# Performance work log

Hardware: AMD Instinct MI355X
Metric: run time of the kernel (lower is better)

## Reference

```python
import jax, jax.numpy as jnp
import numpy as np

B, S, D, H, K = 16, 4096, 256, 512, 3
EPS = 1e-5


def setup_inputs() -> dict:
    key = jax.random.key(0)
    ks = jax.random.split(key, 16)
    glorot = lambda k, shape: jax.random.uniform(
        k, shape, jnp.float32, -1.0, 1.0) * np.sqrt(6.0 / (shape[0] + shape[-1]))
    return {
        "inputs": jax.random.normal(ks[0], (B, S, D), jnp.float32),
        "mask": jax.random.randint(ks[1], (B, S), 0, 2, jnp.int32),
        "in_w": glorot(ks[2], (H, D)),
        "in_b": jnp.zeros((H,), jnp.float32),
        "gate_w": glorot(ks[3], (H, D)),
        "gate_b": jnp.zeros((H,), jnp.float32),
        "dw_w": glorot(ks[4], (H, 1, K)),
        "dw_b": jnp.zeros((H,), jnp.float32),
        "pw_w": glorot(ks[5], (H, H, 1)),
        "pw_b": jnp.zeros((H,), jnp.float32),
        "ln_g": jnp.ones((H,), jnp.float32),
        "ln_b": jnp.zeros((H,), jnp.float32),
        "A_log": jax.random.normal(ks[6], (H,), jnp.float32) * -0.1,
        "Bp": jax.random.normal(ks[7], (H,), jnp.float32) * 0.1,
        "Cp": jax.random.normal(ks[8], (H,), jnp.float32) * 0.1,
    }


def _forward(inputs, mask, in_w, in_b, gate_w, gate_b, dw_w, dw_b,
             pw_w, pw_b, ln_g, ln_b, A_log, Bp, Cp):
    # projections: torch Linear is x @ W.T + b
    x_lin = jnp.einsum('bsd,hd->bsh', inputs, in_w) + in_b
    g_lin = jnp.einsum('bsd,hd->bsh', inputs, gate_w) + gate_b
    h = jnp.tanh(x_lin)
    m_f = mask.astype(h.dtype)                      # [B,S]
    h = h * m_f[:, :, None]
    # depthwise conv over time: [B,H,S] with groups=H, 'same' padding
    pad = (K - 1) // 2
    h_t = jnp.transpose(h, (0, 2, 1))               # [B,H,S]
    h_conv = jax.lax.conv_general_dilated(
        h_t, dw_w, window_strides=(1,), padding=[(pad, pad)],
        dimension_numbers=('NCH', 'OIH', 'NCH'), feature_group_count=H)
    h_conv = h_conv + dw_b[None, :, None]
    h_conv = jnp.transpose(h_conv, (0, 2, 1))       # [B,S,H]
    # pointwise 1x1 conv
    h_conv = jnp.einsum('bsh,oh->bso', h_conv, pw_w[:, :, 0]) + pw_b
    u = jax.nn.silu(h_conv + h)
    g = jax.nn.sigmoid(g_lin)
    a_exp = jnp.exp(-jax.nn.softplus(A_log))        # [H]

    def step(carry, xs):
        state, last = carry
        ut, gt, mt = xs                             # [B,H],[B,H],[B]
        new_state = gt * (a_exp * state) + (1.0 - gt) * (Bp * ut)
        keep = (mt > 0.5)[:, None]
        state = jnp.where(keep, new_state, state)
        y = state * Cp
        last = jnp.where(keep, y, last)
        return (state, last), last

    init = (jnp.zeros((B, H), u.dtype), jnp.zeros((B, H), u.dtype))
    xs = (jnp.transpose(u, (1, 0, 2)), jnp.transpose(g, (1, 0, 2)),
          jnp.transpose(m_f, (1, 0)))
    _, y_seq = jax.lax.scan(step, init, xs)         # [S,B,H]
    y_seq = jnp.transpose(y_seq, (1, 0, 2))         # [B,S,H]
    # LayerNorm over last dim
    mu = jnp.mean(y_seq, axis=-1, keepdims=True)
    var = jnp.var(y_seq, axis=-1, keepdims=True)
    return (y_seq - mu) * jax.lax.rsqrt(var + EPS) * ln_g + ln_b


def reference(inputs, mask, in_w, in_b, gate_w, gate_b, dw_w, dw_b,
              pw_w, pw_b, ln_g, ln_b, A_log, Bp, Cp):
    return _forward(inputs, mask, in_w, in_b, gate_w, gate_b, dw_w, dw_b,
                    pw_w, pw_b, ln_g, ln_b, A_log, Bp, Cp)
```

## Files before the change

### kernel.cpp

```cpp
#include <hip/hip_runtime.h>
#include <hip/hip_bf16.h>
#include <math.h>

#define B_  16
#define S_  4096
#define D_  256
#define H_  512
#define BS_ 65536
#define BSH_ 33554432L
#define BSD_ 16777216L
#define CCH 128
#define LCH 32
#define TPAD 136

typedef __bf16 bf16;
typedef __bf16 bf16x8 __attribute__((ext_vector_type(8)));
typedef float  f32x4  __attribute__((ext_vector_type(4)));

#define AS1 __attribute__((address_space(1)))
#define AS3 __attribute__((address_space(3)))

__device__ __forceinline__ void gload_lds16(const void* g, void* l) {
  __builtin_amdgcn_global_load_lds((const AS1 void*)g, (AS3 void*)l, 16, 0, 0);
}

#if __has_builtin(__builtin_amdgcn_exp2f)
#define EXP2F __builtin_amdgcn_exp2f
#else
#define EXP2F exp2f
#endif
#if __has_builtin(__builtin_amdgcn_rcpf)
#define RCPF __builtin_amdgcn_rcpf
#else
#define RCPF(x) (1.f/(x))
#endif
#define L2E 1.4426950408889634f

__device__ __forceinline__ float fsigmoid(float x) {
  return RCPF(1.f + EXP2F(-L2E * x));
}
__device__ __forceinline__ float ftanh(float x) {
  return 2.f * RCPF(1.f + EXP2F(-2.f * L2E * x)) - 1.f;
}
__device__ __forceinline__ float fsilu(float x) {
  return x * RCPF(1.f + EXP2F(-L2E * x));
}

__global__ void k_cast_x(const float* __restrict__ x, bf16* __restrict__ xb, int n8) {
  int i = blockIdx.x * blockDim.x + threadIdx.x;
  if (i >= n8) return;
  const float4* p = (const float4*)x + (long)i * 2;
  float4 a = p[0], b = p[1];
  bf16x8 o;
  o[0]=(bf16)a.x; o[1]=(bf16)a.y; o[2]=(bf16)a.z; o[3]=(bf16)a.w;
  o[4]=(bf16)b.x; o[5]=(bf16)b.y; o[6]=(bf16)b.z; o[7]=(bf16)b.w;
  ((bf16x8*)xb)[i] = o;
}

__global__ void k_cast_w(const float* __restrict__ in_w, const float* __restrict__ gate_w,
                         const float* __restrict__ pw_w,
                         bf16* __restrict__ w1, bf16* __restrict__ pw) {
  int i = blockIdx.x * blockDim.x + threadIdx.x;
  const int HD = H_ * D_;
  if (i < HD)            w1[i] = (bf16)in_w[i];
  else if (i < 2 * HD)   w1[i] = (bf16)gate_w[i - HD];
  else {
    int j = i - 2 * HD;
    if (j < H_ * H_)     pw[j] = (bf16)pw_w[j];
  }
}

template<int KDIM, int EPI>
__global__ __launch_bounds__(256)
void k_gemm(const bf16* __restrict__ A, const bf16* __restrict__ Bw,
            const int* __restrict__ mask,
            const float* __restrict__ bias0, const float* __restrict__ bias1,
            const bf16* __restrict__ hbuf,
            bf16* __restrict__ out0, bf16* __restrict__ out1, int Ntiles)
{
  extern __shared__ char smem_raw[];
  bf16* As_ = (bf16*)smem_raw;
  bf16* Bs_ = (bf16*)smem_raw + 3 * 4096;
  bf16* tile = (bf16*)smem_raw;

  const int t = threadIdx.x;
  const int w = t >> 6, lane = t & 63;
  const int nwg = gridDim.x;
  const int wg = (blockIdx.x & 7) * (nwg >> 3) + (blockIdx.x >> 3);
  const int bn0 = (wg % Ntiles) * 128;
  const int bm0 = (wg / Ntiles) * 128;
  const int wm = w >> 1, wn = w & 1;
  const int srow = t >> 2;
  const int skoff = (t & 3) * 8;
  const int fr = lane & 15, kq = lane >> 4;
  constexpr int NT = KDIM / 32;

  f32x4 acc[4][4];
#pragma unroll
  for (int i = 0; i < 4; ++i)
#pragma unroll
    for (int j = 0; j < 4; ++j) acc[i][j] = (f32x4){0.f, 0.f, 0.f, 0.f};

#define STAGE(tt)                                                              \
  {                                                                            \
    const int _bi = (tt) % 3;                                                  \
    _Pragma("unroll")                                                          \
    for (int i = 0; i < 2; ++i) {                                              \
      gload_lds16(A  + (long)(bm0 + i * 64 + srow) * KDIM + (tt) * 32 + skoff, \
                  As_ + _bi * 4096 + i * 2048 + t * 8);                        \
      gload_lds16(Bw + (long)(bn0 + i * 64 + srow) * KDIM + (tt) * 32 + skoff, \
                  Bs_ + _bi * 4096 + i * 2048 + t * 8);                        \
    }                                                                          \
  }

  STAGE(0); STAGE(1); STAGE(2);

#pragma unroll
  for (int kt = 0; kt < NT; ++kt) {
    if (kt + 2 < NT)      asm volatile("s_waitcnt vmcnt(8)" ::: "memory");
    else if (kt + 1 < NT) asm volatile("s_waitcnt vmcnt(4)" ::: "memory");
    else                  asm volatile("s_waitcnt vmcnt(0)" ::: "memory");
    __builtin_amdgcn_s_barrier();

    const bf16* As = As_ + (kt % 3) * 4096;
    const bf16* Bs = Bs_ + (kt % 3) * 4096;
    bf16x8 af[4], bfr[4];
#pragma unroll
    for (int mi = 0; mi < 4; ++mi)
      af[mi] = *(const bf16x8*)&As[(wm * 64 + mi * 16 + fr) * 32 + kq * 8];
#pragma unroll
    for (int ni = 0; ni < 4; ++ni)
      bfr[ni] = *(const bf16x8*)&Bs[(wn * 64 + ni * 16 + fr) * 32 + kq * 8];

    asm volatile("s_waitcnt lgkmcnt(0)" ::: "memory");
    __builtin_amdgcn_s_barrier();

    if (kt + 3 < NT) STAGE(kt + 3);

#pragma unroll
    for (int mi = 0; mi < 4; ++mi)
#pragma unroll
      for (int ni = 0; ni < 4; ++ni)
        acc[mi][ni] = __builtin_amdgcn_mfma_f32_16x16x32_bf16(af[mi], bfr[ni], acc[mi][ni], 0, 0, 0);
  }
#undef STAGE

  const bool hside = (EPI != 1) || (bn0 < H_);
#pragma unroll
  for (int mi = 0; mi < 4; ++mi) {
#pragma unroll
    for (int rr = 0; rr < 4; ++rr) {
      const int row = wm * 64 + mi * 16 + kq * 4 + rr;
      const int gm = bm0 + row;
      float mf = 1.f;
      if (EPI == 1) mf = (mask[gm] != 0) ? 1.f : 0.f;
#pragma unroll
      for (int ni = 0; ni < 4; ++ni) {
        const int col = wn * 64 + ni * 16 + fr;
        float c = acc[mi][ni][rr];
        float val;
        if (EPI == 1) {
          const int gn = bn0 + col;
          val = hside ? ftanh(c + bias0[gn]) * mf
                      : fsigmoid(c + bias1[gn - H_]);
        } else {
          val = c + bias0[bn0 + col];
        }
        tile[row * TPAD + col] = (bf16)val;
      }
    }
  }
  __syncthreads();

  const int pr = t >> 4;
  const int pc = (t & 15) * 8;
#pragma unroll
  for (int rr = 0; rr < 8; ++rr) {
    const int row = pr + rr * 16;
    const long gm = bm0 + row;
    bf16x8 v = *(const bf16x8*)&tile[row * TPAD + pc];
    if (EPI == 1) {
      if (hside) *(bf16x8*)&out0[gm * H_ + bn0 + pc] = v;
      else       *(bf16x8*)&out1[gm * H_ + (bn0 - H_) + pc] = v;
    } else {
      bf16x8 hb = *(const bf16x8*)&hbuf[gm * H_ + bn0 + pc];
      bf16x8 o;
#pragma unroll
      for (int k = 0; k < 8; ++k) {
        float s = (float)v[k] + (float)hb[k];
        o[k] = (bf16)fsilu(s);
      }
      *(bf16x8*)&out0[gm * H_ + bn0 + pc] = o;
    }
  }
}

__global__ void k_dwconv(const bf16* __restrict__ h, const float* __restrict__ dww,
                         const float* __restrict__ dwb, bf16* __restrict__ hc)
{
  long idx = (long)blockIdx.x * blockDim.x + threadIdx.x;
  long m = idx >> 6;
  int h8 = ((int)idx & 63) << 3;
  int s = (int)(m & (S_ - 1));
  bf16x8 c0, c1, c2;
#pragma unroll
  for (int j = 0; j < 8; ++j) { c0[j] = (bf16)0.f; c2[j] = (bf16)0.f; }
  if (s > 0)        c0 = *(const bf16x8*)(h + (m - 1) * H_ + h8);
  c1 = *(const bf16x8*)(h + m * H_ + h8);
  if (s < S_ - 1)   c2 = *(const bf16x8*)(h + (m + 1) * H_ + h8);
  bf16x8 o;
#pragma unroll
  for (int j = 0; j < 8; ++j) {
    int hh = h8 + j;
    float v = (float)c0[j] * dww[hh * 3 + 0] + (float)c1[j] * dww[hh * 3 + 1]
            + (float)c2[j] * dww[hh * 3 + 2] + dwb[hh];
    o[j] = (bf16)v;
  }
  *(bf16x8*)(hc + m * H_ + h8) = o;
}


__global__ __launch_bounds__(512)
void k_scan1(const bf16* __restrict__ u, const bf16* __restrict__ g,
             const int* __restrict__ mask, const float* __restrict__ A_log,
             const float* __restrict__ Bp,
             float* __restrict__ Ac, float* __restrict__ Bc)
{
  int c = blockIdx.x, b = blockIdx.y, h = threadIdx.x;
  float aexp = 1.f / (1.f + expf(A_log[h]));
  float bp = Bp[h];
  float At = 1.f, Bt = 0.f;
  long base = ((long)b * S_ + (long)c * LCH) * H_ + h;
  const int* mrow = mask + b * S_ + c * LCH;
  for (int sl = 0; sl < LCH; ++sl) {
    float uv = (float)u[base + (long)sl * H_];
    float gv = (float)g[base + (long)sl * H_];
    bool mm = mrow[sl] != 0;
    float a_s = mm ? gv * aexp : 1.f;
    float b_s = mm ? (1.f - gv) * (bp * uv) : 0.f;
    At = a_s * At;
    Bt = fmaf(a_s, Bt, b_s);
  }
  long o = ((long)c * B_ + b) * H_ + h;
  Ac[o] = At; Bc[o] = Bt;
}

__global__ __launch_bounds__(256)
void k_scan2(const float* __restrict__ Ac, const float* __restrict__ Bc,
             float* __restrict__ Sin)
{
  int tid = blockIdx.x * 256 + threadIdx.x;
  int b = tid >> 9, h = tid & (H_ - 1);
  const long stride = (long)B_ * H_;
  long o = (long)b * H_ + h;
  float st = 0.f;
  float a = Ac[o], bb = Bc[o];
  for (int c = 0; c < CCH; ++c) {
    float an = 0.f, bn = 0.f;
    if (c + 1 < CCH) { an = Ac[o + stride]; bn = Bc[o + stride]; }
    Sin[o] = st;
    st = fmaf(a, st, bb);
    a = an; bb = bn; o += stride;
  }
}

__global__ __launch_bounds__(512)
void k_scan3(const bf16* __restrict__ u, const bf16* __restrict__ g,
             const int* __restrict__ mask, const float* __restrict__ A_log,
             const float* __restrict__ Bp, const float* __restrict__ Cp,
             const float* __restrict__ Sin,
             const float* __restrict__ ln_g, const float* __restrict__ ln_b,
             float* __restrict__ out)
{
  __shared__ float ylds[LCH][H_];
  int c = blockIdx.x, b = blockIdx.y, h = threadIdx.x;
  float aexp = 1.f / (1.f + expf(A_log[h]));
  float bp = Bp[h], cp = Cp[h];
  float st = Sin[((long)c * B_ + b) * H_ + h];
  long base = ((long)b * S_ + (long)c * LCH) * H_ + h;
  const int* mrow = mask + b * S_ + c * LCH;
  for (int sl = 0; sl < LCH; ++sl) {
    float uv = (float)u[base + (long)sl * H_];
    float gv = (float)g[base + (long)sl * H_];
    bool mm = mrow[sl] != 0;
    float a_s = mm ? gv * aexp : 1.f;
    float b_s = mm ? (1.f - gv) * (bp * uv) : 0.f;
    st = fmaf(a_s, st, b_s);
    ylds[sl][h] = st * cp;
  }
  __syncthreads();
  int wv = h >> 6, ln = h & 63;
#pragma unroll
  for (int rr = 0; rr < 4; ++rr) {
    int row = wv * 4 + rr;
    float v[8];
    float sum = 0.f, sq = 0.f;
#pragma unroll
    for (int j = 0; j < 8; ++j) {
      v[j] = ylds[row][ln + 64 * j];
      sum += v[j]; sq += v[j] * v[j];
    }
#pragma unroll
    for (int off = 32; off; off >>= 1) {
      sum += __shfl_xor(sum, off);
      sq  += __shfl_xor(sq, off);
    }
    float mu = sum * (1.f / H_);
    float var = sq * (1.f / H_) - mu * mu;
    float rs = rsqrtf(var + 1e-5f);
    long ob = ((long)b * S_ + (long)c * LCH + row) * H_;
#pragma unroll
    for (int j = 0; j < 8; ++j) {
      int col = ln + 64 * j;
      out[ob + col] = (v[j] - mu) * rs * ln_g[col] + ln_b[col];
    }
  }
}

extern "C" void kernel_launch(void* const* d_in, const int* in_sizes, int n_in,
                              void* d_out, int out_size, void* d_ws, size_t ws_size,
                              hipStream_t stream)
{
  const float* x      = (const float*)d_in[0];
  const int*   mask   = (const int*)d_in[1];
  const float* in_w   = (const float*)d_in[2];
  const float* in_b   = (const float*)d_in[3];
  const float* gate_w = (const float*)d_in[4];
  const float* gate_b = (const float*)d_in[5];
  const float* dw_w   = (const float*)d_in[6];
  const float* dw_b   = (const float*)d_in[7];
  const float* pw_w   = (const float*)d_in[8];
  const float* pw_b   = (const float*)d_in[9];
  const float* ln_g   = (const float*)d_in[10];
  const float* ln_b   = (const float*)d_in[11];
  const float* A_log  = (const float*)d_in[12];
  const float* Bp     = (const float*)d_in[13];
  const float* Cp     = (const float*)d_in[14];

  char* ws = (char*)d_ws;
  bf16*  xb  = (bf16*)(ws + 0L);
  bf16*  h   = (bf16*)(ws + 33554432L);
  bf16*  hc  = (bf16*)(ws + 100663296L);
  bf16*  u   = (bf16*)(ws + 167772160L);
  bf16*  g   = (bf16*)(ws + 234881024L);
  bf16*  w1  = (bf16*)(ws + 301989888L);
  bf16*  pw  = (bf16*)(ws + 302514176L);
  float* Ac  = (float*)(ws + 303038464L);
  float* Bc  = (float*)(ws + 307232768L);
  float* Sin = (float*)(ws + 311427072L);
  float* out = (float*)d_out;

  const int gemm_lds = 3 * 2 * 8192;

  k_cast_x<<<8192, 256, 0, stream>>>(x, xb, (int)(BSD_ / 8));
  k_cast_w<<<2048, 256, 0, stream>>>(in_w, gate_w, pw_w, w1, pw);
  k_gemm<256, 1><<<512 * 8, 256, gemm_lds, stream>>>(xb, w1, mask, in_b, gate_b, nullptr, h, g, 8);
  k_dwconv<<<16384, 256, 0, stream>>>(h, dw_w, dw_b, hc);
  k_gemm<512, 2><<<512 * 4, 256, gemm_lds, stream>>>(hc, pw, nullptr, pw_b, nullptr, h, u, nullptr, 4);
  k_scan1<<<dim3(CCH, B_), 512, 0, stream>>>(u, g, mask, A_log, Bp, Ac, Bc);
  k_scan2<<<32, 256, 0, stream>>>(Ac, Bc, Sin);
  k_scan3<<<dim3(CCH, B_), 512, 0, stream>>>(u, g, mask, A_log, Bp, Cp, Sin, ln_g, ln_b, out);
}
```

Before: 373.6 us.

## Fuse chunk-scan pass into pointwise GEMM epilogue and use 512-thread GEMM blocks

The per-chunk scan reduction (k_scan1) now runs inside the epilogue of the second GEMM. It reads u from the LDS tile and g from global memory, and writes each chunk's Ac/Bc, so the separate scan kernel and its re-read of u are gone. The GEMM also moves to 512 threads with 8 waves, each wave computing a 64x32 subtile. Staging drops from triple to double buffering, with one 16-byte load per operand per thread. This trades a little pipelining depth and per-wave reuse for more waves in flight and one fewer kernel launch and pass over memory.

```diff
diff --git a/kernel.cpp b/kernel.cpp
--- a/kernel.cpp
+++ b/kernel.cpp
@@ -71,16 +71,16 @@
 }
 
 template<int KDIM, int EPI>
-__global__ __launch_bounds__(256)
+__global__ __launch_bounds__(512, 5)
 void k_gemm(const bf16* __restrict__ A, const bf16* __restrict__ Bw,
             const int* __restrict__ mask,
             const float* __restrict__ bias0, const float* __restrict__ bias1,
-            const bf16* __restrict__ hbuf,
+            const bf16* __restrict__ hbuf, const bf16* __restrict__ gbuf,
+            const float* __restrict__ A_log, const float* __restrict__ Bp,
+            float* __restrict__ Ac, float* __restrict__ Bc,
             bf16* __restrict__ out0, bf16* __restrict__ out1, int Ntiles)
 {
   extern __shared__ char smem_raw[];
-  bf16* As_ = (bf16*)smem_raw;
-  bf16* Bs_ = (bf16*)smem_raw + 3 * 4096;
   bf16* tile = (bf16*)smem_raw;
 
   const int t = threadIdx.x;
@@ -89,61 +89,56 @@
   const int wg = (blockIdx.x & 7) * (nwg >> 3) + (blockIdx.x >> 3);
   const int bn0 = (wg % Ntiles) * 128;
   const int bm0 = (wg / Ntiles) * 128;
-  const int wm = w >> 1, wn = w & 1;
-  const int srow = t >> 2;
-  const int skoff = (t & 3) * 8;
+  const int wm = w >> 2, wn = w & 3;
   const int fr = lane & 15, kq = lane >> 4;
   constexpr int NT = KDIM / 32;
 
-  f32x4 acc[4][4];
+  const bf16* Ag = A  + (long)(bm0 + (t >> 2)) * KDIM + (t & 3) * 8;
+  const bf16* Bg = Bw + (long)(bn0 + (t >> 2)) * KDIM + (t & 3) * 8;
+
+  f32x4 acc[4][2];
 #pragma unroll
   for (int i = 0; i < 4; ++i)
 #pragma unroll
-    for (int j = 0; j < 4; ++j) acc[i][j] = (f32x4){0.f, 0.f, 0.f, 0.f};
-
-#define STAGE(tt)                                                              \
-  {                                                                            \
-    const int _bi = (tt) % 3;                                                  \
-    _Pragma("unroll")                                                          \
-    for (int i = 0; i < 2; ++i) {                                              \
-      gload_lds16(A  + (long)(bm0 + i * 64 + srow) * KDIM + (tt) * 32 + skoff, \
-                  As_ + _bi * 4096 + i * 2048 + t * 8);                        \
-      gload_lds16(Bw + (long)(bn0 + i * 64 + srow) * KDIM + (tt) * 32 + skoff, \
-                  Bs_ + _bi * 4096 + i * 2048 + t * 8);                        \
-    }                                                                          \
-  }
-
-  STAGE(0); STAGE(1); STAGE(2);
+    for (int j = 0; j < 2; ++j) acc[i][j] = (f32x4){0.f, 0.f, 0.f, 0.f};
+
+#define STAGE(tt)                                                           \
+  { char* _b = smem_raw + ((tt) & 1) * 16384;                               \
+    gload_lds16(Ag + (tt) * 32, (bf16*)_b + t * 8);                         \
+    gload_lds16(Bg + (tt) * 32, (bf16*)(_b + 8192) + t * 8); }
+
+  STAGE(0); STAGE(1);
 
 #pragma unroll
   for (int kt = 0; kt < NT; ++kt) {
-    if (kt + 2 < NT)      asm volatile("s_waitcnt vmcnt(8)" ::: "memory");
-    else if (kt + 1 < NT) asm volatile("s_waitcnt vmcnt(4)" ::: "memory");
-    else                  asm volatile("s_waitcnt vmcnt(0)" ::: "memory");
+    if (kt + 1 < NT) asm volatile("s_waitcnt vmcnt(2)" ::: "memory");
+    else             asm volatile("s_waitcnt vmcnt(0)" ::: "memory");
     __builtin_amdgcn_s_barrier();
 
-    const bf16* As = As_ + (kt % 3) * 4096;
-    const bf16* Bs = Bs_ + (kt % 3) * 4096;
-    bf16x8 af[4], bfr[4];
+    const bf16* As = (const bf16*)(smem_raw + (kt & 1) * 16384);
+    const bf16* Bs = As + 4096;
+    bf16x8 af[4], bfr[2];
 #pragma unroll
     for (int mi = 0; mi < 4; ++mi)
       af[mi] = *(const bf16x8*)&As[(wm * 64 + mi * 16 + fr) * 32 + kq * 8];
 #pragma unroll
-    for (int ni = 0; ni < 4; ++ni)
-      bfr[ni] = *(const bf16x8*)&Bs[(wn * 64 + ni * 16 + fr) * 32 + kq * 8];
+    for (int ni = 0; ni < 2; ++ni)
+      bfr[ni] = *(const bf16x8*)&Bs[(wn * 32 + ni * 16 + fr) * 32 + kq * 8];
 
     asm volatile("s_waitcnt lgkmcnt(0)" ::: "memory");
     __builtin_amdgcn_s_barrier();
 
-    if (kt + 3 < NT) STAGE(kt + 3);
+    if (kt + 2 < NT) STAGE(kt + 2);
 
 #pragma unroll
     for (int mi = 0; mi < 4; ++mi)
 #pragma unroll
-      for (int ni = 0; ni < 4; ++ni)
+      for (int ni = 0; ni < 2; ++ni)
         acc[mi][ni] = __builtin_amdgcn_mfma_f32_16x16x32_bf16(af[mi], bfr[ni], acc[mi][ni], 0, 0, 0);
   }
 #undef STAGE
+
+  __syncthreads();
 
   const bool hside = (EPI != 1) || (bn0 < H_);
 #pragma unroll
@@ -155,8 +150,8 @@
       float mf = 1.f;
       if (EPI == 1) mf = (mask[gm] != 0) ? 1.f : 0.f;
 #pragma unroll
-      for (int ni = 0; ni < 4; ++ni) {
-        const int col = wn * 64 + ni * 16 + fr;
+      for (int ni = 0; ni < 2; ++ni) {
+        const int col = wn * 32 + ni * 16 + fr;
         float c = acc[mi][ni][rr];
         float val;
         if (EPI == 1) {
@@ -175,8 +170,8 @@
   const int pr = t >> 4;
   const int pc = (t & 15) * 8;
 #pragma unroll
-  for (int rr = 0; rr < 8; ++rr) {
-    const int row = pr + rr * 16;
+  for (int rr = 0; rr < 4; ++rr) {
+    const int row = pr + rr * 32;
     const long gm = bm0 + row;
     bf16x8 v = *(const bf16x8*)&tile[row * TPAD + pc];
     if (EPI == 1) {
@@ -191,7 +186,35 @@
         o[k] = (bf16)fsilu(s);
       }
       *(bf16x8*)&out0[gm * H_ + bn0 + pc] = o;
-    }
+      *(bf16x8*)&tile[row * TPAD + pc] = o;
+    }
+  }
+
+  if constexpr (EPI == 2) {
+    __syncthreads();
+    const int c_idx = t >> 7;
+    const int col   = t & 127;
+    const int gcol  = bn0 + col;
+    const int bIdx  = bm0 >> 12;
+    const int s0    = bm0 & (S_ - 1);
+    const int chunk = (s0 >> 5) + c_idx;
+    const int* mrow = mask + bIdx * S_ + s0 + c_idx * 32;
+    const float aexp = RCPF(1.f + EXP2F(L2E * A_log[gcol]));
+    const float bp = Bp[gcol];
+    const bf16* grow = gbuf + (long)(bm0 + c_idx * 32) * H_ + gcol;
+    float At = 1.f, Bt = 0.f;
+#pragma unroll 4
+    for (int sl = 0; sl < LCH; ++sl) {
+      float uv = (float)tile[(c_idx * 32 + sl) * TPAD + col];
+      float gv = (float)grow[(long)sl * H_];
+      bool mm = mrow[sl] != 0;
+      float a_s = mm ? gv * aexp : 1.f;
+      float b_s = mm ? (1.f - gv) * (bp * uv) : 0.f;
+      At = a_s * At;
+      Bt = fmaf(a_s, Bt, b_s);
+    }
+    long o = ((long)chunk * B_ + bIdx) * H_ + gcol;
+    Ac[o] = At; Bc[o] = Bt;
   }
 }
 
@@ -219,31 +242,6 @@
   *(bf16x8*)(hc + m * H_ + h8) = o;
 }
 
-
-__global__ __launch_bounds__(512)
-void k_scan1(const bf16* __restrict__ u, const bf16* __restrict__ g,
-             const int* __restrict__ mask, const float* __restrict__ A_log,
-             const float* __restrict__ Bp,
-             float* __restrict__ Ac, float* __restrict__ Bc)
-{
-  int c = blockIdx.x, b = blockIdx.y, h = threadIdx.x;
-  float aexp = 1.f / (1.f + expf(A_log[h]));
-  float bp = Bp[h];
-  float At = 1.f, Bt = 0.f;
-  long base = ((long)b * S_ + (long)c * LCH) * H_ + h;
-  const int* mrow = mask + b * S_ + c * LCH;
-  for (int sl = 0; sl < LCH; ++sl) {
-    float uv = (float)u[base + (long)sl * H_];
-    float gv = (float)g[base + (long)sl * H_];
-    bool mm = mrow[sl] != 0;
-    float a_s = mm ? gv * aexp : 1.f;
-    float b_s = mm ? (1.f - gv) * (bp * uv) : 0.f;
-    At = a_s * At;
-    Bt = fmaf(a_s, Bt, b_s);
-  }
-  long o = ((long)c * B_ + b) * H_ + h;
-  Ac[o] = At; Bc[o] = Bt;
-}
 
 __global__ __launch_bounds__(256)
 void k_scan2(const float* __restrict__ Ac, const float* __restrict__ Bc,
@@ -350,14 +348,17 @@
   float* Sin = (float*)(ws + 311427072L);
   float* out = (float*)d_out;
 
-  const int gemm_lds = 3 * 2 * 8192;
+  const int gemm_lds = 128 * TPAD * 2;
 
   k_cast_x<<<8192, 256, 0, stream>>>(x, xb, (int)(BSD_ / 8));
   k_cast_w<<<2048, 256, 0, stream>>>(in_w, gate_w, pw_w, w1, pw);
-  k_gemm<256, 1><<<512 * 8, 256, gemm_lds, stream>>>(xb, w1, mask, in_b, gate_b, nullptr, h, g, 8);
+  k_gemm<256, 1><<<512 * 8, 512, gemm_lds, stream>>>(
+      xb, w1, mask, in_b, gate_b, nullptr, nullptr, nullptr, nullptr,
+      nullptr, nullptr, h, g, 8);
   k_dwconv<<<16384, 256, 0, stream>>>(h, dw_w, dw_b, hc);
-  k_gemm<512, 2><<<512 * 4, 256, gemm_lds, stream>>>(hc, pw, nullptr, pw_b, nullptr, h, u, nullptr, 4);
-  k_scan1<<<dim3(CCH, B_), 512, 0, stream>>>(u, g, mask, A_log, Bp, Ac, Bc);
+  k_gemm<512, 2><<<512 * 4, 512, gemm_lds, stream>>>(
+      hc, pw, mask, pw_b, nullptr, h, g, A_log, Bp,
+      Ac, Bc, u, nullptr, 4);
   k_scan2<<<32, 256, 0, stream>>>(Ac, Bc, Sin);
   k_scan3<<<dim3(CCH, B_), 512, 0, stream>>>(u, g, mask, A_log, Bp, Cp, Sin, ln_g, ln_b, out);
 }
```

After: 375.4 us. Within noise of the previous version (+0.5%).
